# Kernel tuning notes

Hardware: AMD Instinct MI355X
Metric: run time of the kernel (lower is better)

## Reference

```python
import jax, jax.numpy as jnp
import numpy as np

N = 10000
E = 160000
D_IN = 128
H = 1024
NUM_GRAPHS = 8
EPS = 1e-5


def setup_inputs() -> dict:
    key = jax.random.key(0)
    ks = jax.random.split(key, 24)
    x = jax.random.normal(ks[0], (N, D_IN), dtype=jnp.float32)
    edge_index = jax.random.randint(ks[1], (2, E), 0, N, dtype=jnp.int32)
    batch = jnp.sort(jax.random.randint(ks[2], (N,), 0, NUM_GRAPHS, dtype=jnp.int32))
    s = 0.02
    W1 = jax.random.normal(ks[3], (D_IN, H), dtype=jnp.float32) * s
    b1 = jnp.zeros((H,), jnp.float32)
    Wh = jax.random.normal(ks[4], (3, H, H), dtype=jnp.float32) * s
    bh = jnp.zeros((3, H), jnp.float32)
    ln_g = jnp.ones((4, H), jnp.float32)
    ln_b = jnp.zeros((4, H), jnp.float32)
    vW = jax.random.normal(ks[5], (6, H, H), dtype=jnp.float32) * s
    vb = jnp.zeros((6, H), jnp.float32)
    vWo = jax.random.normal(ks[6], (H, 1), dtype=jnp.float32) * s
    vbo = jnp.zeros((1,), jnp.float32)
    return {"x": x, "edge_index": edge_index, "batch": batch,
            "W1": W1, "b1": b1, "Wh": Wh, "bh": bh,
            "ln_g": ln_g, "ln_b": ln_b, "vW": vW, "vb": vb,
            "vWo": vWo, "vbo": vbo}


def _layer_norm(x, g, b):
    m = jnp.mean(x, axis=-1, keepdims=True)
    v = jnp.mean(jnp.square(x - m), axis=-1, keepdims=True)
    return (x - m) * jax.lax.rsqrt(v + EPS) * g + b


def reference(x, edge_index, batch, W1, b1, Wh, bh, ln_g, ln_b, vW, vb, vWo, vbo):
    # GCNConv: add self loops, symmetric normalization, x @ W, scatter-add at dst, + bias
    loops = jnp.arange(N, dtype=edge_index.dtype)
    src = jnp.concatenate([edge_index[0], loops])
    dst = jnp.concatenate([edge_index[1], loops])
    deg = jax.ops.segment_sum(jnp.ones_like(dst, dtype=x.dtype), dst, num_segments=N)
    dinv = jax.lax.rsqrt(jnp.maximum(deg, 1.0))
    norm = (dinv[src] * dinv[dst])[:, None]  # [E+N, 1]

    def gcn(h, W, b):
        h = h @ W                              # [N, H]
        msg = h[src] * norm                    # gather + scale [E+N, H]
        return jax.ops.segment_sum(msg, dst, num_segments=N) + b

    x1 = gcn(x, W1, b1)
    h = jax.nn.relu(_layer_norm(x1, ln_g[0], ln_b[0]))
    x2 = gcn(h, Wh[0], bh[0])
    h = jax.nn.relu(_layer_norm(x2 + x1, ln_g[1], ln_b[1]))
    x3 = gcn(h, Wh[1], bh[1])
    h = jax.nn.relu(_layer_norm(x3 + x1, ln_g[2], ln_b[2]))
    x4 = gcn(h, Wh[2], bh[2])
    node_embeddings = jax.nn.relu(_layer_norm(x4 + h, ln_g[3], ln_b[3]))

    # global mean pool per graph
    counts = jax.ops.segment_sum(jnp.ones((N,), x.dtype), batch, num_segments=NUM_GRAPHS)
    sums = jax.ops.segment_sum(node_embeddings, batch, num_segments=NUM_GRAPHS)
    graph_embedding = sums / jnp.maximum(counts, 1.0)[:, None]

    v = graph_embedding
    for i in range(6):
        v = jax.nn.relu(v @ vW[i] + vb[i])
    state_value = (v @ vWo + vbo).squeeze(-1)
    return node_embeddings, graph_embedding, state_value
```

## Files before the change

kernel.cpp:

```cpp
#include <hip/hip_runtime.h>
#include <stdint.h>

#define N_NODES 10000
#define E_EDGES 160000
#define DIN 128
#define H 1024
#define NUM_GRAPHS 8
#define LN_EPS 1e-5f

typedef unsigned short u16;
typedef __attribute__((ext_vector_type(8))) short short8;
typedef __attribute__((ext_vector_type(8))) unsigned short ushort8v;
typedef __attribute__((ext_vector_type(4))) float f32x4;

__device__ __forceinline__ float bf2f(u16 v) { return __uint_as_float(((unsigned)v) << 16); }
__device__ __forceinline__ u16 f2bf(float f) {
    unsigned u = __float_as_uint(f);
    u += 0x7fffu + ((u >> 16) & 1u);
    return (u16)(u >> 16);
}

__global__ void k_init(int* cnt, int* goff, float* __restrict__ gsum,
                       float* __restrict__ vbuf, const float* __restrict__ vb) {
    int i = blockIdx.x * 256 + threadIdx.x;
    if (i < N_NODES) cnt[i] = 0;
    if (i <= NUM_GRAPHS) goff[i] = 0;
    if (i < NUM_GRAPHS * H) gsum[i] = 0.f;
    if (i < 6 * H) {
        int il = i >> 10, j = i & (H - 1);
        float b = vb[il * H + j];
        float* base = vbuf + (size_t)(il + 1) * NUM_GRAPHS * H;
#pragma unroll
        for (int g = 0; g < NUM_GRAPHS; g++) base[g * H + j] = b;
    }
}

__global__ void k_count(const int* __restrict__ dst, int* __restrict__ cnt) {
    int e = blockIdx.x * 256 + threadIdx.x;
    if (e < E_EDGES) atomicAdd(&cnt[dst[e]], 1);
}

__global__ __launch_bounds__(1024) void k_scan(const int* __restrict__ cnt, int* __restrict__ offs,
                                               int* __restrict__ cursor, float* __restrict__ dinv) {
    __shared__ int wsum[16];
    __shared__ int carry_s;
    int tid = threadIdx.x;
    int lane = tid & 63, wv = tid >> 6;
    if (tid == 0) carry_s = 0;
    __syncthreads();
    for (int base = 0; base < N_NODES; base += 1024) {
        int i = base + tid;
        int v = (i < N_NODES) ? cnt[i] : 0;
        int x = v;
#pragma unroll
        for (int off = 1; off < 64; off <<= 1) {
            int t = __shfl_up(x, off);
            if (lane >= off) x += t;
        }
        if (lane == 63) wsum[wv] = x;
        __syncthreads();
        int carry = carry_s;
        if (wv == 0) {
            int ws = (lane < 16) ? wsum[lane] : 0;
#pragma unroll
            for (int off = 1; off < 16; off <<= 1) {
                int t = __shfl_up(ws, off);
                if (lane >= off) ws += t;
            }
            if (lane < 16) wsum[lane] = ws;
        }
        __syncthreads();
        int wbase = (wv > 0) ? wsum[wv - 1] : 0;
        int incl = wbase + x;
        int excl = incl - v;
        if (i < N_NODES) {
            offs[i] = carry + excl;
            cursor[i] = carry + excl;
            dinv[i] = rsqrtf((float)(v + 1));
        }
        if (tid == 1023) carry_s = carry + incl;
        __syncthreads();
    }
    if (tid == 0) offs[N_NODES] = carry_s;
}

__global__ void k_fill(const int* __restrict__ src, const int* __restrict__ dst,
                       int* __restrict__ cursor, int* __restrict__ csr_src) {
    int e = blockIdx.x * 256 + threadIdx.x;
    if (e < E_EDGES) {
        int d = dst[e];
        int slot = atomicAdd(&cursor[d], 1);
        csr_src[slot] = src[e];
    }
}

__global__ void k_gbound(const int* __restrict__ batch, int* __restrict__ goff) {
    int i = blockIdx.x * 256 + threadIdx.x;
    if (i >= N_NODES) return;
    int b0 = batch[i];
    int b1 = (i + 1 < N_NODES) ? batch[i + 1] : NUM_GRAPHS;
    for (int g = b0 + 1; g <= b1; g++) goff[g] = i + 1;
}

__global__ void k_cvt(const float* __restrict__ src, u16* __restrict__ dst, int n) {
    int i = blockIdx.x * 256 + threadIdx.x;
    if (i < n) dst[i] = f2bf(src[i]);
}

__global__ void k_transpose_cvt(const float* __restrict__ src0, u16* __restrict__ dst0, int R, int C) {
    __shared__ float tile[32][33];
    const float* src = src0 + (size_t)blockIdx.z * R * C;
    u16* dst = dst0 + (size_t)blockIdx.z * R * C;
    int tx = threadIdx.x, ty = threadIdx.y;
    int x = blockIdx.x * 32 + tx;
#pragma unroll
    for (int i = 0; i < 32; i += 8) {
        int y = blockIdx.y * 32 + ty + i;
        tile[ty + i][tx] = (y < R && x < C) ? src[(size_t)y * C + x] : 0.f;
    }
    __syncthreads();
    int xo = blockIdx.y * 32 + tx;
#pragma unroll
    for (int i = 0; i < 32; i += 8) {
        int yo = blockIdx.x * 32 + ty + i;
        if (yo < C && xo < R) dst[(size_t)yo * R + xo] = f2bf(tile[tx][ty + i]);
    }
}

__global__ __launch_bounds__(64) void k_agg_x(const u16* __restrict__ xb, const float* __restrict__ dinv,
                                              const int* __restrict__ offs, const int* __restrict__ csr_src,
                                              u16* __restrict__ xa) {
    __shared__ float s_dv[64];
    __shared__ int s_id[64];
    int d = blockIdx.x;
    int tid = threadIdx.x;
    int c = tid * 2;
    float dd = dinv[d];
    float a0, a1;
    {
        unsigned v = *(const unsigned*)(xb + (size_t)d * DIN + c);
        a0 = dd * bf2f((u16)(v & 0xffffu));
        a1 = dd * bf2f((u16)(v >> 16));
    }
    int beg = offs[d], end = offs[d + 1];
    for (int chunk = beg; chunk < end; chunk += 64) {
        int nthis = end - chunk;
        if (nthis > 64) nthis = 64;
        int np = (nthis + 7) & ~7;
        __syncthreads();
        if (tid < nthis) {
            int s = csr_src[chunk + tid];
            s_id[tid] = s;
            s_dv[tid] = dinv[s];
        } else if (tid < np) {
            s_id[tid] = d;
            s_dv[tid] = 0.f;
        }
        __syncthreads();
        for (int i = 0; i < np; i += 8) {
            unsigned v[8];
            float e[8];
#pragma unroll
            for (int u = 0; u < 8; u++) {
                int s = s_id[i + u];
                e[u] = s_dv[i + u];
                v[u] = *(const unsigned*)(xb + (size_t)s * DIN + c);
            }
#pragma unroll
            for (int u = 0; u < 8; u++) {
                a0 += e[u] * bf2f((u16)(v[u] & 0xffffu));
                a1 += e[u] * bf2f((u16)(v[u] >> 16));
            }
        }
    }
    a0 *= dd;
    a1 *= dd;
    unsigned o = ((unsigned)f2bf(a1) << 16) | (unsigned)f2bf(a0);
    *(unsigned*)(xa + (size_t)d * DIN + c) = o;
}

__global__ __launch_bounds__(256) void k_agg_col(const u16* __restrict__ t, const float* __restrict__ dinv,
                                                 const int* __restrict__ offs, const int* __restrict__ csr_src,
                                                 u16* __restrict__ abuf) {
    int chunk = blockIdx.x & 7;
    int grp = threadIdx.x >> 4;
    int ln = threadIdx.x & 15;
    int d = (blockIdx.x >> 3) * 16 + grp;
    size_t col = (size_t)chunk * 128 + (size_t)ln * 8;
    const u16* tc = t + col;
    float dd = dinv[d];
    float a[8];
    {
        ushort8v v = *(const ushort8v*)(tc + (size_t)d * H);
#pragma unroll
        for (int i = 0; i < 8; i++) a[i] = dd * bf2f(v[i]);
    }
    int e = offs[d], end = offs[d + 1];
    for (; e + 4 <= end; e += 4) {
        int s0 = csr_src[e], s1 = csr_src[e + 1], s2 = csr_src[e + 2], s3 = csr_src[e + 3];
        float w0 = dinv[s0], w1 = dinv[s1], w2 = dinv[s2], w3 = dinv[s3];
        ushort8v v0 = *(const ushort8v*)(tc + (size_t)s0 * H);
        ushort8v v1 = *(const ushort8v*)(tc + (size_t)s1 * H);
        ushort8v v2 = *(const ushort8v*)(tc + (size_t)s2 * H);
        ushort8v v3 = *(const ushort8v*)(tc + (size_t)s3 * H);
#pragma unroll
        for (int j = 0; j < 8; j++)
            a[j] += w0 * bf2f(v0[j]) + w1 * bf2f(v1[j]) + w2 * bf2f(v2[j]) + w3 * bf2f(v3[j]);
    }
    for (; e < end; e++) {
        int s0 = csr_src[e];
        float w0 = dinv[s0];
        ushort8v v0 = *(const ushort8v*)(tc + (size_t)s0 * H);
#pragma unroll
        for (int j = 0; j < 8; j++) a[j] += w0 * bf2f(v0[j]);
    }
    ushort8v o;
#pragma unroll
    for (int i = 0; i < 8; i++) o[i] = f2bf(dd * a[i]);
    __builtin_nontemporal_store(o, (ushort8v*)(abuf + (size_t)d * H + col));
}

template <int MODE>
__global__ __launch_bounds__(128) void k_ln(const u16* __restrict__ a, const u16* __restrict__ resid,
                                            const float* __restrict__ bias, const float* __restrict__ gamma,
                                            const float* __restrict__ beta,
                                            u16* __restrict__ out_bf, u16* __restrict__ out_pre,
                                            float* __restrict__ out_f32) {
    __shared__ float red1[2], red2[2];
    int d = blockIdx.x;
    int tid = threadIdx.x;
    int c = tid * 8;
    float x[8];
    {
        ushort8v v = *(const ushort8v*)(a + (size_t)d * H + c);
#pragma unroll
        for (int i = 0; i < 8; i++) x[i] = bf2f(v[i]) + bias[c + i];
    }
    if (MODE >= 1) {
        ushort8v r = *(const ushort8v*)(resid + (size_t)d * H + c);
#pragma unroll
        for (int i = 0; i < 8; i++) x[i] += bf2f(r[i]);
    }
    if (MODE == 0) {
        ushort8v p;
#pragma unroll
        for (int i = 0; i < 8; i++) p[i] = f2bf(x[i]);
        *(ushort8v*)(out_pre + (size_t)d * H + c) = p;
    }
    float s1 = 0.f, s2 = 0.f;
#pragma unroll
    for (int i = 0; i < 8; i++) { s1 += x[i]; s2 += x[i] * x[i]; }
#pragma unroll
    for (int off = 32; off > 0; off >>= 1) {
        s1 += __shfl_down(s1, off);
        s2 += __shfl_down(s2, off);
    }
    int lane = tid & 63, wv = tid >> 6;
    if (lane == 0) { red1[wv] = s1; red2[wv] = s2; }
    __syncthreads();
    float sum = red1[0] + red1[1];
    float ssq = red2[0] + red2[1];
    float mean = sum * (1.f / H);
    float var = fmaxf(ssq * (1.f / H) - mean * mean, 0.f);
    float inv = rsqrtf(var + LN_EPS);
    float y[8];
#pragma unroll
    for (int i = 0; i < 8; i++)
        y[i] = fmaxf((x[i] - mean) * inv * gamma[c + i] + beta[c + i], 0.f);
    if (MODE == 2) {
        float4 o0 = {y[0], y[1], y[2], y[3]};
        float4 o1 = {y[4], y[5], y[6], y[7]};
        *(float4*)(out_f32 + (size_t)d * H + c) = o0;
        *(float4*)(out_f32 + (size_t)d * H + c + 4) = o1;
    } else {
        ushort8v o;
#pragma unroll
        for (int i = 0; i < 8; i++) o[i] = f2bf(y[i]);
        *(ushort8v*)(out_bf + (size_t)d * H + c) = o;
    }
}

typedef __attribute__((address_space(1))) const unsigned int gas_u32;
typedef __attribute__((address_space(3))) unsigned int las_u32;
__device__ __forceinline__ void gld_lds16(const void* g, void* l) {
    __builtin_amdgcn_global_load_lds((gas_u32*)g, (las_u32*)l, 16, 0, 0);
}

__global__ __launch_bounds__(256) void k_gemm(const u16* __restrict__ A, const u16* __restrict__ B,
                                              u16* __restrict__ C, int M, int Nn, int K) {
    __shared__ __align__(16) u16 sA[2][128 * 32];
    __shared__ __align__(16) u16 sB[2][128 * 32];
    int mtiles = (M + 127) >> 7;
    int L = blockIdx.x;
    int cls = L & 7;
    int s = L >> 3;
    int nt = s & 7;
    int mt = (s >> 3) * 8 + cls;
    if (mt >= mtiles) return;
    int m0 = mt << 7;
    int n0 = nt << 7;

    int tid = threadIdx.x;
    int lane = tid & 63;
    int w = tid >> 6;
    int wm = w >> 1, wn = w & 1;

    f32x4 zero = {0.f, 0.f, 0.f, 0.f};
    f32x4 acc[4][4];
#pragma unroll
    for (int i = 0; i < 4; i++)
#pragma unroll
        for (int j = 0; j < 4; j++) acc[i][j] = zero;

    int srow = w * 32 + (lane >> 2);
    int scol = (((lane & 3) ^ ((lane >> 3) & 3))) * 8;

    auto STAGE = [&](int p, int k0) {
#pragma unroll
        for (int q = 0; q < 2; q++) {
            int rA = m0 + srow + q * 16;
            rA = rA < M ? rA : M - 1;
            gld_lds16(A + (size_t)rA * K + k0 + scol, sA[p] + w * 1024 + q * 512);
            gld_lds16(B + (size_t)(n0 + srow + q * 16) * K + k0 + scol, sB[p] + w * 1024 + q * 512);
        }
    };

    int NK = K >> 5;
    STAGE(0, 0);
    __syncthreads();

    int rchunk = ((lane >> 4) ^ ((lane >> 1) & 3)) * 8;
    int arow = (wm * 64 + (lane & 15)) * 32 + rchunk;
    int brow = (wn * 64 + (lane & 15)) * 32 + rchunk;

    for (int kt = 0; kt < NK; kt++) {
        int cur = kt & 1;
        if (kt + 1 < NK) STAGE(cur ^ 1, (kt + 1) << 5);

        short8 af[4], bv[4];
#pragma unroll
        for (int mi = 0; mi < 4; mi++)
            af[mi] = *(const short8*)(sA[cur] + arow + mi * 16 * 32);
#pragma unroll
        for (int ni = 0; ni < 4; ni++)
            bv[ni] = *(const short8*)(sB[cur] + brow + ni * 16 * 32);
#pragma unroll
        for (int mi = 0; mi < 4; mi++)
#pragma unroll
            for (int ni = 0; ni < 4; ni++)
                acc[mi][ni] = __builtin_amdgcn_mfma_f32_16x16x32_bf16(af[mi], bv[ni], acc[mi][ni], 0, 0, 0);

        __syncthreads();
    }

    int rbase = m0 + wm * 64 + (lane >> 4) * 4;
    int cbase = n0 + wn * 64 + (lane & 15);
#pragma unroll
    for (int mi = 0; mi < 4; mi++) {
#pragma unroll
        for (int r = 0; r < 4; r++) {
            int row = rbase + mi * 16 + r;
            if (row < M) {
#pragma unroll
                for (int ni = 0; ni < 4; ni++)
                    C[(size_t)row * Nn + cbase + ni * 16] = f2bf(acc[mi][ni][r]);
            }
        }
    }
}

#define PC_NODES 16
__global__ __launch_bounds__(256) void k_pool_acc(const float* __restrict__ ne, const int* __restrict__ batch,
                                                  float* __restrict__ gsum) {
    int c = blockIdx.x * 256 + threadIdx.x;
    int nbeg = blockIdx.y * PC_NODES;
    int nend = nbeg + PC_NODES;
    if (nend > N_NODES) nend = N_NODES;
    float acc = 0.f;
    int curg = batch[nbeg];
    for (int n = nbeg; n < nend; n++) {
        int g = batch[n];
        if (g != curg) {
            atomicAdd(&gsum[curg * H + c], acc);
            acc = 0.f;
            curg = g;
        }
        acc += ne[(size_t)n * H + c];
    }
    atomicAdd(&gsum[curg * H + c], acc);
}

__global__ __launch_bounds__(256) void k_pool_fin(const float* __restrict__ gsum, const int* __restrict__ goff,
                                                  float* __restrict__ v0, float* __restrict__ ge_out) {
    int g = blockIdx.y;
    int c = blockIdx.x * 256 + threadIdx.x;
    float cntf = (float)(goff[g + 1] - goff[g]);
    float m = gsum[g * H + c] / fmaxf(cntf, 1.f);
    v0[g * H + c] = m;
    ge_out[(size_t)g * H + c] = m;
}

template <bool RELU_IN>
__global__ __launch_bounds__(256) void k_mlp_acc(const float* __restrict__ vin, const float* __restrict__ W,
                                                 float* __restrict__ vout) {
    __shared__ float sk[64];
    int g = blockIdx.y;
    int j = blockIdx.x * 256 + threadIdx.x;
    int k0 = blockIdx.z * 64;
    if (threadIdx.x < 64) {
        float v = vin[g * H + k0 + threadIdx.x];
        sk[threadIdx.x] = RELU_IN ? fmaxf(v, 0.f) : v;
    }
    __syncthreads();
    float acc = 0.f;
#pragma unroll
    for (int k = 0; k < 64; k++) acc += sk[k] * W[(size_t)(k0 + k) * H + j];
    atomicAdd(&vout[g * H + j], acc);
}

__global__ void k_head(const float* __restrict__ vin, const float* __restrict__ Wo,
                       const float* __restrict__ bo, float* __restrict__ out) {
    int g = blockIdx.x;
    int tid = threadIdx.x;
    float s = 0.f;
    for (int k = tid; k < H; k += 256) s += fmaxf(vin[g * H + k], 0.f) * Wo[k];
#pragma unroll
    for (int off = 32; off > 0; off >>= 1) s += __shfl_down(s, off);
    __shared__ float p[4];
    if ((tid & 63) == 0) p[tid >> 6] = s;
    __syncthreads();
    if (tid == 0) out[g] = p[0] + p[1] + p[2] + p[3] + bo[0];
}

extern "C" void kernel_launch(void* const* d_in, const int* in_sizes, int n_in,
                              void* d_out, int out_size, void* d_ws, size_t ws_size,
                              hipStream_t stream) {
    const float* x = (const float*)d_in[0];
    const int* ei = (const int*)d_in[1];
    const int* batch = (const int*)d_in[2];
    const float* W1 = (const float*)d_in[3];
    const float* b1 = (const float*)d_in[4];
    const float* Wh = (const float*)d_in[5];
    const float* bh = (const float*)d_in[6];
    const float* ln_g = (const float*)d_in[7];
    const float* ln_b = (const float*)d_in[8];
    const float* vW = (const float*)d_in[9];
    const float* vb = (const float*)d_in[10];
    const float* vWo = (const float*)d_in[11];
    const float* vbo = (const float*)d_in[12];
    const int* esrc = ei;
    const int* edst = ei + E_EDGES;

    char* ws = (char*)d_ws;
    size_t off = 0;
    auto carve = [&](size_t bytes) -> char* {
        char* p = ws + off;
        off += (bytes + 255) & ~(size_t)255;
        return p;
    };
    float* dinv = (float*)carve(N_NODES * 4);
    int* cnt = (int*)carve(N_NODES * 4);
    int* offs = (int*)carve((N_NODES + 1) * 4);
    int* cursor = (int*)carve(N_NODES * 4);
    int* csr_src = (int*)carve(E_EDGES * 4);
    int* goff = (int*)carve((NUM_GRAPHS + 1) * 4);
    float* gsum = (float*)carve(NUM_GRAPHS * H * 4);
    float* vbuf = (float*)carve((size_t)7 * NUM_GRAPHS * H * 4);
    u16* xb = (u16*)carve((size_t)N_NODES * DIN * 2);
    u16* xa = (u16*)carve((size_t)N_NODES * DIN * 2);
    u16* Wt1 = (u16*)carve((size_t)H * DIN * 2);
    u16* Wt3 = (u16*)carve((size_t)3 * H * H * 2);
    u16* tbuf = (u16*)carve((size_t)N_NODES * H * 2);
    u16* hbuf = (u16*)carve((size_t)N_NODES * H * 2);
    u16* x1buf = (u16*)carve((size_t)N_NODES * H * 2);
    u16* abuf = (u16*)carve((size_t)N_NODES * H * 2);

    float* out_ne = (float*)d_out;
    float* out_ge = out_ne + (size_t)N_NODES * H;
    float* out_sv = out_ge + (size_t)NUM_GRAPHS * H;

    k_init<<<(N_NODES + 255) / 256, 256, 0, stream>>>(cnt, goff, gsum, vbuf, vb);
    k_count<<<(E_EDGES + 255) / 256, 256, 0, stream>>>(edst, cnt);
    k_scan<<<1, 1024, 0, stream>>>(cnt, offs, cursor, dinv);
    k_fill<<<(E_EDGES + 255) / 256, 256, 0, stream>>>(esrc, edst, cursor, csr_src);
    k_gbound<<<(N_NODES + 255) / 256, 256, 0, stream>>>(batch, goff);
    k_cvt<<<(N_NODES * DIN + 255) / 256, 256, 0, stream>>>(x, xb, N_NODES * DIN);

    dim3 tb(32, 8);
    int mtiles = (N_NODES + 127) / 128;
    int gemm_grid = 8 * 8 * ((mtiles + 7) / 8);
    int agg_grid = (N_NODES / 16) * 8;

    k_transpose_cvt<<<dim3(H / 32, DIN / 32, 1), tb, 0, stream>>>(W1, Wt1, DIN, H);
    k_transpose_cvt<<<dim3(H / 32, H / 32, 3), tb, 0, stream>>>(Wh, Wt3, H, H);

    k_agg_x<<<N_NODES, 64, 0, stream>>>(xb, dinv, offs, csr_src, xa);
    k_gemm<<<gemm_grid, 256, 0, stream>>>(xa, Wt1, tbuf, N_NODES, H, DIN);
    k_ln<0><<<N_NODES, 128, 0, stream>>>(tbuf, nullptr, b1, ln_g, ln_b, hbuf, x1buf, nullptr);

    k_gemm<<<gemm_grid, 256, 0, stream>>>(hbuf, Wt3, tbuf, N_NODES, H, H);
    k_agg_col<<<agg_grid, 256, 0, stream>>>(tbuf, dinv, offs, csr_src, abuf);
    k_ln<1><<<N_NODES, 128, 0, stream>>>(abuf, x1buf, bh, ln_g + H, ln_b + H, hbuf, nullptr, nullptr);

    k_gemm<<<gemm_grid, 256, 0, stream>>>(hbuf, Wt3 + (size_t)H * H, tbuf, N_NODES, H, H);
    k_agg_col<<<agg_grid, 256, 0, stream>>>(tbuf, dinv, offs, csr_src, abuf);
    k_ln<1><<<N_NODES, 128, 0, stream>>>(abuf, x1buf, bh + H, ln_g + 2 * H, ln_b + 2 * H, hbuf, nullptr, nullptr);

    k_gemm<<<gemm_grid, 256, 0, stream>>>(hbuf, Wt3 + (size_t)2 * H * H, tbuf, N_NODES, H, H);
    k_agg_col<<<agg_grid, 256, 0, stream>>>(tbuf, dinv, offs, csr_src, abuf);
    k_ln<2><<<N_NODES, 128, 0, stream>>>(abuf, hbuf, bh + 2 * H, ln_g + 3 * H, ln_b + 3 * H, nullptr, nullptr, out_ne);

    k_pool_acc<<<dim3(H / 256, (N_NODES + PC_NODES - 1) / PC_NODES), 256, 0, stream>>>(out_ne, batch, gsum);
    k_pool_fin<<<dim3(H / 256, NUM_GRAPHS), 256, 0, stream>>>(gsum, goff, vbuf, out_ge);

    dim3 mg(H / 256, NUM_GRAPHS, 16);
    k_mlp_acc<false><<<mg, 256, 0, stream>>>(vbuf, vW, vbuf + (size_t)1 * NUM_GRAPHS * H);
    for (int i = 1; i < 6; i++)
        k_mlp_acc<true><<<mg, 256, 0, stream>>>(vbuf + (size_t)i * NUM_GRAPHS * H, vW + (size_t)i * H * H,
                                                vbuf + (size_t)(i + 1) * NUM_GRAPHS * H);
    k_head<<<NUM_GRAPHS, 256, 0, stream>>>(vbuf + (size_t)6 * NUM_GRAPHS * H, vWo, vbo, out_sv);
}
```

Before: 445.7 us.

## Fuse bias, residual and LayerNorm statistics into aggregation; merge setup kernels

The aggregation kernel now adds bias and residual, stores the pre-norm sum, and accumulates per-node sum and sum-of-squares with atomics. A lightweight apply kernel then normalizes using those statistics, so the residual read and a separate block-wide reduction pass go away. Several small setup kernels (count, graph bounds, x conversion, weight transposes) are merged into fewer launches, and the gather loop is unrolled to 8 edges. The trade-offs are extra atomic traffic and the one-pass E[x^2]-mean^2 variance taken from bf16-rounded intermediates.

```diff
diff --git a/kernel.cpp b/kernel.cpp
--- a/kernel.cpp
+++ b/kernel.cpp
@@ -21,7 +21,8 @@
 }
 
 __global__ void k_init(int* cnt, int* goff, float* __restrict__ gsum,
-                       float* __restrict__ vbuf, const float* __restrict__ vb) {
+                       float* __restrict__ vbuf, const float* __restrict__ vb,
+                       float* __restrict__ sbufs) {
     int i = blockIdx.x * 256 + threadIdx.x;
     if (i < N_NODES) cnt[i] = 0;
     if (i <= NUM_GRAPHS) goff[i] = 0;
@@ -33,11 +34,20 @@
 #pragma unroll
         for (int g = 0; g < NUM_GRAPHS; g++) base[g * H + j] = b;
     }
-}
-
-__global__ void k_count(const int* __restrict__ dst, int* __restrict__ cnt) {
-    int e = blockIdx.x * 256 + threadIdx.x;
-    if (e < E_EDGES) atomicAdd(&cnt[dst[e]], 1);
+    for (int j = i; j < 3 * N_NODES * 2; j += 40 * 256) sbufs[j] = 0.f;
+}
+
+__global__ void k_setup(const int* __restrict__ dst, int* __restrict__ cnt,
+                        const int* __restrict__ batch, int* __restrict__ goff,
+                        const float* __restrict__ x, u16* __restrict__ xb) {
+    int i = blockIdx.x * 256 + threadIdx.x;
+    if (i < E_EDGES) atomicAdd(&cnt[dst[i]], 1);
+    if (i < N_NODES) {
+        int b0 = batch[i];
+        int b1 = (i + 1 < N_NODES) ? batch[i + 1] : NUM_GRAPHS;
+        for (int g = b0 + 1; g <= b1; g++) goff[g] = i + 1;
+    }
+    if (i < N_NODES * DIN) xb[i] = f2bf(x[i]);
 }
 
 __global__ __launch_bounds__(1024) void k_scan(const int* __restrict__ cnt, int* __restrict__ offs,
@@ -94,23 +104,22 @@
     }
 }
 
-__global__ void k_gbound(const int* __restrict__ batch, int* __restrict__ goff) {
-    int i = blockIdx.x * 256 + threadIdx.x;
-    if (i >= N_NODES) return;
-    int b0 = batch[i];
-    int b1 = (i + 1 < N_NODES) ? batch[i + 1] : NUM_GRAPHS;
-    for (int g = b0 + 1; g <= b1; g++) goff[g] = i + 1;
-}
-
-__global__ void k_cvt(const float* __restrict__ src, u16* __restrict__ dst, int n) {
-    int i = blockIdx.x * 256 + threadIdx.x;
-    if (i < n) dst[i] = f2bf(src[i]);
-}
-
-__global__ void k_transpose_cvt(const float* __restrict__ src0, u16* __restrict__ dst0, int R, int C) {
+__global__ void k_wprep(const float* __restrict__ W1, const float* __restrict__ Wh,
+                        u16* __restrict__ Wt1, u16* __restrict__ Wt3) {
     __shared__ float tile[32][33];
-    const float* src = src0 + (size_t)blockIdx.z * R * C;
-    u16* dst = dst0 + (size_t)blockIdx.z * R * C;
+    int z = blockIdx.z;
+    const float* src;
+    u16* dst;
+    int R;
+    if (z == 0) {
+        if (blockIdx.y * 32 >= DIN) return;
+        src = W1; dst = Wt1; R = DIN;
+    } else {
+        src = Wh + (size_t)(z - 1) * H * H;
+        dst = Wt3 + (size_t)(z - 1) * H * H;
+        R = H;
+    }
+    const int C = H;
     int tx = threadIdx.x, ty = threadIdx.y;
     int x = blockIdx.x * 32 + tx;
 #pragma unroll
@@ -179,69 +188,20 @@
     *(unsigned*)(xa + (size_t)d * DIN + c) = o;
 }
 
-__global__ __launch_bounds__(256) void k_agg_col(const u16* __restrict__ t, const float* __restrict__ dinv,
-                                                 const int* __restrict__ offs, const int* __restrict__ csr_src,
-                                                 u16* __restrict__ abuf) {
-    int chunk = blockIdx.x & 7;
-    int grp = threadIdx.x >> 4;
-    int ln = threadIdx.x & 15;
-    int d = (blockIdx.x >> 3) * 16 + grp;
-    size_t col = (size_t)chunk * 128 + (size_t)ln * 8;
-    const u16* tc = t + col;
-    float dd = dinv[d];
-    float a[8];
-    {
-        ushort8v v = *(const ushort8v*)(tc + (size_t)d * H);
-#pragma unroll
-        for (int i = 0; i < 8; i++) a[i] = dd * bf2f(v[i]);
-    }
-    int e = offs[d], end = offs[d + 1];
-    for (; e + 4 <= end; e += 4) {
-        int s0 = csr_src[e], s1 = csr_src[e + 1], s2 = csr_src[e + 2], s3 = csr_src[e + 3];
-        float w0 = dinv[s0], w1 = dinv[s1], w2 = dinv[s2], w3 = dinv[s3];
-        ushort8v v0 = *(const ushort8v*)(tc + (size_t)s0 * H);
-        ushort8v v1 = *(const ushort8v*)(tc + (size_t)s1 * H);
-        ushort8v v2 = *(const ushort8v*)(tc + (size_t)s2 * H);
-        ushort8v v3 = *(const ushort8v*)(tc + (size_t)s3 * H);
-#pragma unroll
-        for (int j = 0; j < 8; j++)
-            a[j] += w0 * bf2f(v0[j]) + w1 * bf2f(v1[j]) + w2 * bf2f(v2[j]) + w3 * bf2f(v3[j]);
-    }
-    for (; e < end; e++) {
-        int s0 = csr_src[e];
-        float w0 = dinv[s0];
-        ushort8v v0 = *(const ushort8v*)(tc + (size_t)s0 * H);
-#pragma unroll
-        for (int j = 0; j < 8; j++) a[j] += w0 * bf2f(v0[j]);
-    }
-    ushort8v o;
-#pragma unroll
-    for (int i = 0; i < 8; i++) o[i] = f2bf(dd * a[i]);
-    __builtin_nontemporal_store(o, (ushort8v*)(abuf + (size_t)d * H + col));
-}
-
-template <int MODE>
-__global__ __launch_bounds__(128) void k_ln(const u16* __restrict__ a, const u16* __restrict__ resid,
-                                            const float* __restrict__ bias, const float* __restrict__ gamma,
-                                            const float* __restrict__ beta,
-                                            u16* __restrict__ out_bf, u16* __restrict__ out_pre,
-                                            float* __restrict__ out_f32) {
+__global__ __launch_bounds__(128) void k_ln1(const u16* __restrict__ t, const float* __restrict__ bias,
+                                             const float* __restrict__ gamma, const float* __restrict__ beta,
+                                             u16* __restrict__ out_bf, u16* __restrict__ out_pre) {
     __shared__ float red1[2], red2[2];
     int d = blockIdx.x;
     int tid = threadIdx.x;
     int c = tid * 8;
     float x[8];
     {
-        ushort8v v = *(const ushort8v*)(a + (size_t)d * H + c);
+        ushort8v v = *(const ushort8v*)(t + (size_t)d * H + c);
 #pragma unroll
         for (int i = 0; i < 8; i++) x[i] = bf2f(v[i]) + bias[c + i];
     }
-    if (MODE >= 1) {
-        ushort8v r = *(const ushort8v*)(resid + (size_t)d * H + c);
-#pragma unroll
-        for (int i = 0; i < 8; i++) x[i] += bf2f(r[i]);
-    }
-    if (MODE == 0) {
+    {
         ushort8v p;
 #pragma unroll
         for (int i = 0; i < 8; i++) p[i] = f2bf(x[i]);
@@ -263,20 +223,113 @@
     float mean = sum * (1.f / H);
     float var = fmaxf(ssq * (1.f / H) - mean * mean, 0.f);
     float inv = rsqrtf(var + LN_EPS);
+    ushort8v o;
+#pragma unroll
+    for (int i = 0; i < 8; i++)
+        o[i] = f2bf(fmaxf((x[i] - mean) * inv * gamma[c + i] + beta[c + i], 0.f));
+    *(ushort8v*)(out_bf + (size_t)d * H + c) = o;
+}
+
+__global__ __launch_bounds__(256) void k_agg_col(const u16* __restrict__ t, const u16* __restrict__ resid,
+                                                 const float* __restrict__ bias, const float* __restrict__ dinv,
+                                                 const int* __restrict__ offs, const int* __restrict__ csr_src,
+                                                 u16* __restrict__ abuf, float* __restrict__ sbuf) {
+    int chunk = blockIdx.x & 7;
+    int grp = threadIdx.x >> 4;
+    int ln = threadIdx.x & 15;
+    int d = (blockIdx.x >> 3) * 16 + grp;
+    int col = chunk * 128 + ln * 8;
+    const u16* tc = t + col;
+    float dd = dinv[d];
+    float a[8];
+    {
+        ushort8v v = *(const ushort8v*)(tc + (size_t)d * H);
+#pragma unroll
+        for (int i = 0; i < 8; i++) a[i] = dd * bf2f(v[i]);
+    }
+    int e = offs[d], end = offs[d + 1];
+    for (; e + 8 <= end; e += 8) {
+        int s[8];
+        float w[8];
+        ushort8v vv[8];
+#pragma unroll
+        for (int u = 0; u < 8; u++) s[u] = csr_src[e + u];
+#pragma unroll
+        for (int u = 0; u < 8; u++) {
+            w[u] = dinv[s[u]];
+            vv[u] = *(const ushort8v*)(tc + (size_t)s[u] * H);
+        }
+#pragma unroll
+        for (int u = 0; u < 8; u++)
+#pragma unroll
+            for (int j = 0; j < 8; j++) a[j] += w[u] * bf2f(vv[u][j]);
+    }
+    for (; e + 2 <= end; e += 2) {
+        int s0 = csr_src[e], s1 = csr_src[e + 1];
+        float w0 = dinv[s0], w1 = dinv[s1];
+        ushort8v v0 = *(const ushort8v*)(tc + (size_t)s0 * H);
+        ushort8v v1 = *(const ushort8v*)(tc + (size_t)s1 * H);
+#pragma unroll
+        for (int j = 0; j < 8; j++) a[j] += w0 * bf2f(v0[j]) + w1 * bf2f(v1[j]);
+    }
+    if (e < end) {
+        int s0 = csr_src[e];
+        float w0 = dinv[s0];
+        ushort8v v0 = *(const ushort8v*)(tc + (size_t)s0 * H);
+#pragma unroll
+        for (int j = 0; j < 8; j++) a[j] += w0 * bf2f(v0[j]);
+    }
+    float x[8];
+    {
+        ushort8v r = *(const ushort8v*)(resid + (size_t)d * H + col);
+#pragma unroll
+        for (int i = 0; i < 8; i++) x[i] = dd * a[i] + bias[col + i] + bf2f(r[i]);
+    }
+    ushort8v o;
+#pragma unroll
+    for (int i = 0; i < 8; i++) o[i] = f2bf(x[i]);
+    *(ushort8v*)(abuf + (size_t)d * H + col) = o;
+    float s1 = 0.f, s2 = 0.f;
+#pragma unroll
+    for (int i = 0; i < 8; i++) { s1 += x[i]; s2 += x[i] * x[i]; }
+#pragma unroll
+    for (int off = 1; off < 16; off <<= 1) {
+        s1 += __shfl_xor(s1, off);
+        s2 += __shfl_xor(s2, off);
+    }
+    if (ln == 0) {
+        atomicAdd(&sbuf[d * 2], s1);
+        atomicAdd(&sbuf[d * 2 + 1], s2);
+    }
+}
+
+template <int MODE>
+__global__ __launch_bounds__(256) void k_ln_apply(const u16* __restrict__ abuf, const float* __restrict__ sbuf,
+                                                  const float* __restrict__ gamma, const float* __restrict__ beta,
+                                                  u16* __restrict__ out_bf, float* __restrict__ out_f32) {
+    int chunk = blockIdx.x & 7;
+    int grp = threadIdx.x >> 4;
+    int ln = threadIdx.x & 15;
+    int d = (blockIdx.x >> 3) * 16 + grp;
+    int col = chunk * 128 + ln * 8;
+    float mean = sbuf[d * 2] * (1.f / H);
+    float var = fmaxf(sbuf[d * 2 + 1] * (1.f / H) - mean * mean, 0.f);
+    float inv = rsqrtf(var + LN_EPS);
+    ushort8v v = *(const ushort8v*)(abuf + (size_t)d * H + col);
     float y[8];
 #pragma unroll
     for (int i = 0; i < 8; i++)
-        y[i] = fmaxf((x[i] - mean) * inv * gamma[c + i] + beta[c + i], 0.f);
+        y[i] = fmaxf((bf2f(v[i]) - mean) * inv * gamma[col + i] + beta[col + i], 0.f);
     if (MODE == 2) {
         float4 o0 = {y[0], y[1], y[2], y[3]};
         float4 o1 = {y[4], y[5], y[6], y[7]};
-        *(float4*)(out_f32 + (size_t)d * H + c) = o0;
-        *(float4*)(out_f32 + (size_t)d * H + c + 4) = o1;
+        *(float4*)(out_f32 + (size_t)d * H + col) = o0;
+        *(float4*)(out_f32 + (size_t)d * H + col + 4) = o1;
     } else {
         ushort8v o;
 #pragma unroll
         for (int i = 0; i < 8; i++) o[i] = f2bf(y[i]);
-        *(ushort8v*)(out_bf + (size_t)d * H + c) = o;
+        *(ushort8v*)(out_bf + (size_t)d * H + col) = o;
     }
 }
 
@@ -466,6 +519,7 @@
     int* goff = (int*)carve((NUM_GRAPHS + 1) * 4);
     float* gsum = (float*)carve(NUM_GRAPHS * H * 4);
     float* vbuf = (float*)carve((size_t)7 * NUM_GRAPHS * H * 4);
+    float* sbufs = (float*)carve((size_t)3 * N_NODES * 2 * 4);
     u16* xb = (u16*)carve((size_t)N_NODES * DIN * 2);
     u16* xa = (u16*)carve((size_t)N_NODES * DIN * 2);
     u16* Wt1 = (u16*)carve((size_t)H * DIN * 2);
@@ -479,36 +533,31 @@
     float* out_ge = out_ne + (size_t)N_NODES * H;
     float* out_sv = out_ge + (size_t)NUM_GRAPHS * H;
 
-    k_init<<<(N_NODES + 255) / 256, 256, 0, stream>>>(cnt, goff, gsum, vbuf, vb);
-    k_count<<<(E_EDGES + 255) / 256, 256, 0, stream>>>(edst, cnt);
+    k_init<<<(N_NODES + 255) / 256, 256, 0, stream>>>(cnt, goff, gsum, vbuf, vb, sbufs);
+    k_setup<<<(N_NODES * DIN + 255) / 256, 256, 0, stream>>>(edst, cnt, batch, goff, x, xb);
     k_scan<<<1, 1024, 0, stream>>>(cnt, offs, cursor, dinv);
     k_fill<<<(E_EDGES + 255) / 256, 256, 0, stream>>>(esrc, edst, cursor, csr_src);
-    k_gbound<<<(N_NODES + 255) / 256, 256, 0, stream>>>(batch, goff);
-    k_cvt<<<(N_NODES * DIN + 255) / 256, 256, 0, stream>>>(x, xb, N_NODES * DIN);
-
-    dim3 tb(32, 8);
+    k_wprep<<<dim3(H / 32, H / 32, 4), dim3(32, 8), 0, stream>>>(W1, Wh, Wt1, Wt3);
+
     int mtiles = (N_NODES + 127) / 128;
     int gemm_grid = 8 * 8 * ((mtiles + 7) / 8);
     int agg_grid = (N_NODES / 16) * 8;
 
-    k_transpose_cvt<<<dim3(H / 32, DIN / 32, 1), tb, 0, stream>>>(W1, Wt1, DIN, H);
-    k_transpose_cvt<<<dim3(H / 32, H / 32, 3), tb, 0, stream>>>(Wh, Wt3, H, H);
-
     k_agg_x<<<N_NODES, 64, 0, stream>>>(xb, dinv, offs, csr_src, xa);
     k_gemm<<<gemm_grid, 256, 0, stream>>>(xa, Wt1, tbuf, N_NODES, H, DIN);
-    k_ln<0><<<N_NODES, 128, 0, stream>>>(tbuf, nullptr, b1, ln_g, ln_b, hbuf, x1buf, nullptr);
+    k_ln1<<<N_NODES, 128, 0, stream>>>(tbuf, b1, ln_g, ln_b, hbuf, x1buf);
 
     k_gemm<<<gemm_grid, 256, 0, stream>>>(hbuf, Wt3, tbuf, N_NODES, H, H);
-    k_agg_col<<<agg_grid, 256, 0, stream>>>(tbuf, dinv, offs, csr_src, abuf);
-    k_ln<1><<<N_NODES, 128, 0, stream>>>(abuf, x1buf, bh, ln_g + H, ln_b + H, hbuf, nullptr, nullptr);
+    k_agg_col<<<agg_grid, 256, 0, stream>>>(tbuf, x1buf, bh, dinv, offs, csr_src, abuf, sbufs);
+    k_ln_apply<1><<<agg_grid, 256, 0, stream>>>(abuf, sbufs, ln_g + H, ln_b + H, hbuf, nullptr);
 
     k_gemm<<<gemm_grid, 256, 0, stream>>>(hbuf, Wt3 + (size_t)H * H, tbuf, N_NODES, H, H);
-    k_agg_col<<<agg_grid, 256, 0, stream>>>(tbuf, dinv, offs, csr_src, abuf);
-    k_ln<1><<<N_NODES, 128, 0, stream>>>(abuf, x1buf, bh + H, ln_g + 2 * H, ln_b + 2 * H, hbuf, nullptr, nullptr);
+    k_agg_col<<<agg_grid, 256, 0, stream>>>(tbuf, x1buf, bh + H, dinv, offs, csr_src, abuf, sbufs + 2 * N_NODES);
+    k_ln_apply<1><<<agg_grid, 256, 0, stream>>>(abuf, sbufs + 2 * N_NODES, ln_g + 2 * H, ln_b + 2 * H, hbuf, nullptr);
 
     k_gemm<<<gemm_grid, 256, 0, stream>>>(hbuf, Wt3 + (size_t)2 * H * H, tbuf, N_NODES, H, H);
-    k_agg_col<<<agg_grid, 256, 0, stream>>>(tbuf, dinv, offs, csr_src, abuf);
-    k_ln<2><<<N_NODES, 128, 0, stream>>>(abuf, hbuf, bh + 2 * H, ln_g + 3 * H, ln_b + 3 * H, nullptr, nullptr, out_ne);
+    k_agg_col<<<agg_grid, 256, 0, stream>>>(tbuf, hbuf, bh + 2 * H, dinv, offs, csr_src, abuf, sbufs + 4 * N_NODES);
+    k_ln_apply<2><<<agg_grid, 256, 0, stream>>>(abuf, sbufs + 4 * N_NODES, ln_g + 3 * H, ln_b + 3 * H, nullptr, out_ne);
 
     k_pool_acc<<<dim3(H / 256, (N_NODES + PC_NODES - 1) / PC_NODES), 256, 0, stream>>>(out_ne, batch, gsum);
     k_pool_fin<<<dim3(H / 256, NUM_GRAPHS), 256, 0, stream>>>(gsum, goff, vbuf, out_ge);
```

Measured after the change: 466.9 us. +4.8%, slower.

## Sort nodes by degree for aggregation balance and fuse setup kernels

Applied to the files above, without the earlier changes.

The scan kernel now builds a permutation of nodes bucketed by in-degree (a counting sort in shared memory), and the column aggregation kernel uses it so each block handles nodes of similar degree. This is meant to reduce divergence and load imbalance among the 16 node groups inside a block. Separately, the edge count, graph-boundary and input-conversion kernels are fused into one launch, and the two weight transpose launches are merged into one. The cost is an extra serial pass in the single-block scan, and the permuted order loses locality in the destination rows.

```diff
diff --git a/kernel.cpp b/kernel.cpp
--- a/kernel.cpp
+++ b/kernel.cpp
@@ -35,22 +35,35 @@
     }
 }
 
-__global__ void k_count(const int* __restrict__ dst, int* __restrict__ cnt) {
-    int e = blockIdx.x * 256 + threadIdx.x;
-    if (e < E_EDGES) atomicAdd(&cnt[dst[e]], 1);
+__global__ void k_setup(const int* __restrict__ dst, int* __restrict__ cnt,
+                        const int* __restrict__ batch, int* __restrict__ goff,
+                        const float* __restrict__ x, u16* __restrict__ xb) {
+    int i = blockIdx.x * 256 + threadIdx.x;
+    if (i < E_EDGES) atomicAdd(&cnt[dst[i]], 1);
+    if (i < N_NODES) {
+        int b0 = batch[i];
+        int b1 = (i + 1 < N_NODES) ? batch[i + 1] : NUM_GRAPHS;
+        for (int g = b0 + 1; g <= b1; g++) goff[g] = i + 1;
+    }
+    if (i < N_NODES * DIN) xb[i] = f2bf(x[i]);
 }
 
 __global__ __launch_bounds__(1024) void k_scan(const int* __restrict__ cnt, int* __restrict__ offs,
-                                               int* __restrict__ cursor, float* __restrict__ dinv) {
+                                               int* __restrict__ cursor, float* __restrict__ dinv,
+                                               int* __restrict__ perm) {
     __shared__ int wsum[16];
     __shared__ int carry_s;
+    __shared__ int bins[256];
+    __shared__ int binoff[256];
     int tid = threadIdx.x;
     int lane = tid & 63, wv = tid >> 6;
     if (tid == 0) carry_s = 0;
+    if (tid < 256) bins[tid] = 0;
     __syncthreads();
     for (int base = 0; base < N_NODES; base += 1024) {
         int i = base + tid;
         int v = (i < N_NODES) ? cnt[i] : 0;
+        if (i < N_NODES) atomicAdd(&bins[v < 255 ? v : 255], 1);
         int x = v;
 #pragma unroll
         for (int off = 1; off < 64; off <<= 1) {
@@ -82,6 +95,26 @@
         __syncthreads();
     }
     if (tid == 0) offs[N_NODES] = carry_s;
+    if (tid < 256) binoff[tid] = bins[tid];
+    __syncthreads();
+    for (int off = 1; off < 256; off <<= 1) {
+        int t = 0;
+        if (tid < 256 && tid >= off) t = binoff[tid - off];
+        __syncthreads();
+        if (tid < 256) binoff[tid] += t;
+        __syncthreads();
+    }
+    if (tid < 256) bins[tid] = binoff[tid] - bins[tid];
+    __syncthreads();
+    for (int base = 0; base < N_NODES; base += 1024) {
+        int i = base + tid;
+        if (i < N_NODES) {
+            int v = cnt[i];
+            v = v < 255 ? v : 255;
+            int slot = atomicAdd(&bins[v], 1);
+            perm[slot] = i;
+        }
+    }
 }
 
 __global__ void k_fill(const int* __restrict__ src, const int* __restrict__ dst,
@@ -94,23 +127,22 @@
     }
 }
 
-__global__ void k_gbound(const int* __restrict__ batch, int* __restrict__ goff) {
-    int i = blockIdx.x * 256 + threadIdx.x;
-    if (i >= N_NODES) return;
-    int b0 = batch[i];
-    int b1 = (i + 1 < N_NODES) ? batch[i + 1] : NUM_GRAPHS;
-    for (int g = b0 + 1; g <= b1; g++) goff[g] = i + 1;
-}
-
-__global__ void k_cvt(const float* __restrict__ src, u16* __restrict__ dst, int n) {
-    int i = blockIdx.x * 256 + threadIdx.x;
-    if (i < n) dst[i] = f2bf(src[i]);
-}
-
-__global__ void k_transpose_cvt(const float* __restrict__ src0, u16* __restrict__ dst0, int R, int C) {
+__global__ void k_wprep(const float* __restrict__ W1, const float* __restrict__ Wh,
+                        u16* __restrict__ Wt1, u16* __restrict__ Wt3) {
     __shared__ float tile[32][33];
-    const float* src = src0 + (size_t)blockIdx.z * R * C;
-    u16* dst = dst0 + (size_t)blockIdx.z * R * C;
+    int z = blockIdx.z;
+    const float* src;
+    u16* dst;
+    int R;
+    if (z == 0) {
+        if (blockIdx.y * 32 >= DIN) return;
+        src = W1; dst = Wt1; R = DIN;
+    } else {
+        src = Wh + (size_t)(z - 1) * H * H;
+        dst = Wt3 + (size_t)(z - 1) * H * H;
+        R = H;
+    }
+    const int C = H;
     int tx = threadIdx.x, ty = threadIdx.y;
     int x = blockIdx.x * 32 + tx;
 #pragma unroll
@@ -181,12 +213,12 @@
 
 __global__ __launch_bounds__(256) void k_agg_col(const u16* __restrict__ t, const float* __restrict__ dinv,
                                                  const int* __restrict__ offs, const int* __restrict__ csr_src,
-                                                 u16* __restrict__ abuf) {
+                                                 const int* __restrict__ perm, u16* __restrict__ abuf) {
     int chunk = blockIdx.x & 7;
     int grp = threadIdx.x >> 4;
     int ln = threadIdx.x & 15;
-    int d = (blockIdx.x >> 3) * 16 + grp;
-    size_t col = (size_t)chunk * 128 + (size_t)ln * 8;
+    int d = perm[(blockIdx.x >> 3) * 16 + grp];
+    int col = chunk * 128 + ln * 8;
     const u16* tc = t + col;
     float dd = dinv[d];
     float a[8];
@@ -463,6 +495,7 @@
     int* offs = (int*)carve((N_NODES + 1) * 4);
     int* cursor = (int*)carve(N_NODES * 4);
     int* csr_src = (int*)carve(E_EDGES * 4);
+    int* perm = (int*)carve(N_NODES * 4);
     int* goff = (int*)carve((NUM_GRAPHS + 1) * 4);
     float* gsum = (float*)carve(NUM_GRAPHS * H * 4);
     float* vbuf = (float*)carve((size_t)7 * NUM_GRAPHS * H * 4);
@@ -480,34 +513,29 @@
     float* out_sv = out_ge + (size_t)NUM_GRAPHS * H;
 
     k_init<<<(N_NODES + 255) / 256, 256, 0, stream>>>(cnt, goff, gsum, vbuf, vb);
-    k_count<<<(E_EDGES + 255) / 256, 256, 0, stream>>>(edst, cnt);
-    k_scan<<<1, 1024, 0, stream>>>(cnt, offs, cursor, dinv);
+    k_setup<<<(N_NODES * DIN + 255) / 256, 256, 0, stream>>>(edst, cnt, batch, goff, x, xb);
+    k_scan<<<1, 1024, 0, stream>>>(cnt, offs, cursor, dinv, perm);
     k_fill<<<(E_EDGES + 255) / 256, 256, 0, stream>>>(esrc, edst, cursor, csr_src);
-    k_gbound<<<(N_NODES + 255) / 256, 256, 0, stream>>>(batch, goff);
-    k_cvt<<<(N_NODES * DIN + 255) / 256, 256, 0, stream>>>(x, xb, N_NODES * DIN);
-
-    dim3 tb(32, 8);
+    k_wprep<<<dim3(H / 32, H / 32, 4), dim3(32, 8), 0, stream>>>(W1, Wh, Wt1, Wt3);
+
     int mtiles = (N_NODES + 127) / 128;
     int gemm_grid = 8 * 8 * ((mtiles + 7) / 8);
     int agg_grid = (N_NODES / 16) * 8;
 
-    k_transpose_cvt<<<dim3(H / 32, DIN / 32, 1), tb, 0, stream>>>(W1, Wt1, DIN, H);
-    k_transpose_cvt<<<dim3(H / 32, H / 32, 3), tb, 0, stream>>>(Wh, Wt3, H, H);
-
     k_agg_x<<<N_NODES, 64, 0, stream>>>(xb, dinv, offs, csr_src, xa);
     k_gemm<<<gemm_grid, 256, 0, stream>>>(xa, Wt1, tbuf, N_NODES, H, DIN);
     k_ln<0><<<N_NODES, 128, 0, stream>>>(tbuf, nullptr, b1, ln_g, ln_b, hbuf, x1buf, nullptr);
 
     k_gemm<<<gemm_grid, 256, 0, stream>>>(hbuf, Wt3, tbuf, N_NODES, H, H);
-    k_agg_col<<<agg_grid, 256, 0, stream>>>(tbuf, dinv, offs, csr_src, abuf);
+    k_agg_col<<<agg_grid, 256, 0, stream>>>(tbuf, dinv, offs, csr_src, perm, abuf);
     k_ln<1><<<N_NODES, 128, 0, stream>>>(abuf, x1buf, bh, ln_g + H, ln_b + H, hbuf, nullptr, nullptr);
 
     k_gemm<<<gemm_grid, 256, 0, stream>>>(hbuf, Wt3 + (size_t)H * H, tbuf, N_NODES, H, H);
-    k_agg_col<<<agg_grid, 256, 0, stream>>>(tbuf, dinv, offs, csr_src, abuf);
+    k_agg_col<<<agg_grid, 256, 0, stream>>>(tbuf, dinv, offs, csr_src, perm, abuf);
     k_ln<1><<<N_NODES, 128, 0, stream>>>(abuf, x1buf, bh + H, ln_g + 2 * H, ln_b + 2 * H, hbuf, nullptr, nullptr);
 
     k_gemm<<<gemm_grid, 256, 0, stream>>>(hbuf, Wt3 + (size_t)2 * H * H, tbuf, N_NODES, H, H);
-    k_agg_col<<<agg_grid, 256, 0, stream>>>(tbuf, dinv, offs, csr_src, abuf);
+    k_agg_col<<<agg_grid, 256, 0, stream>>>(tbuf, dinv, offs, csr_src, perm, abuf);
     k_ln<2><<<N_NODES, 128, 0, stream>>>(abuf, hbuf, bh + 2 * H, ln_g + 3 * H, ln_b + 3 * H, nullptr, nullptr, out_ne);
 
     k_pool_acc<<<dim3(H / 256, (N_NODES + PC_NODES - 1) / PC_NODES), 256, 0, stream>>>(out_ne, batch, gsum);
```

Measured after the change: 433.9 us (median of 2 runs). -2.6%, faster.
